# Kernel optimization log

Measured on AMD Instinct MI355X. Metric: run time of the kernel, lower is better.

## Reference

```python
import jax, jax.numpy as jnp
import numpy as np
from jax.ops import segment_sum

N_NODES = 50000
N_EDGES = 800000
HIDDEN = 96
N_CLASSES = 10
N_GRAPHS = 64


def gcn_conv(x, W, b, src, dst, num_nodes):
    """PyG GCNConv: symmetric-normalized aggregation with self-loops.
    out = D^{-1/2} (A + I) D^{-1/2} (x W) + b, with D the degree of A + I.
    Self-loop contribution handled analytically instead of appending edges.
    """
    ones = jnp.ones((src.shape[0],), dtype=x.dtype)
    deg = segment_sum(ones, dst, num_segments=num_nodes) + 1.0  # +1 for self-loop
    dinv = jax.lax.rsqrt(deg)
    h = x @ W  # [N, H] small GEMM
    norm = dinv[src] * dinv[dst]  # [E]
    msg = h[src] * norm[:, None]  # [E, H] dominant gather
    out = segment_sum(msg, dst, num_segments=num_nodes)  # scatter-add
    out = out + h * (dinv * dinv)[:, None]  # self-loop term
    return out + b


def setup_inputs() -> dict:
    key = jax.random.key(0)
    ks = jax.random.split(key, 12)
    x = jax.random.normal(ks[0], (N_NODES, HIDDEN), dtype=jnp.float32)
    edge_index = jax.random.randint(ks[1], (2, N_EDGES), 0, N_NODES, dtype=jnp.int64)
    batch = jnp.sort(jax.random.randint(ks[2], (N_NODES,), 0, N_GRAPHS, dtype=jnp.int64))
    s = 1.0 / np.sqrt(HIDDEN)
    W0 = jax.random.normal(ks[3], (HIDDEN, HIDDEN), dtype=jnp.float32) * s
    b0 = jnp.zeros((HIDDEN,), dtype=jnp.float32)
    W1 = jax.random.normal(ks[4], (HIDDEN, HIDDEN), dtype=jnp.float32) * s
    b1 = jnp.zeros((HIDDEN,), dtype=jnp.float32)
    W2 = jax.random.normal(ks[5], (HIDDEN, HIDDEN), dtype=jnp.float32) * s
    b2 = jnp.zeros((HIDDEN,), dtype=jnp.float32)
    W_lin = jax.random.normal(ks[6], (HIDDEN, N_CLASSES), dtype=jnp.float32) * s
    b_lin = jnp.zeros((N_CLASSES,), dtype=jnp.float32)
    return {"x": x, "edge_index": edge_index, "batch": batch,
            "W0": W0, "b0": b0, "W1": W1, "b1": b1, "W2": W2, "b2": b2,
            "W_lin": W_lin, "b_lin": b_lin}


def reference(x, edge_index, batch, W0, b0, W1, b1, W2, b2, W_lin, b_lin):
    src, dst = edge_index[0], edge_index[1]
    n = x.shape[0]
    h = jax.nn.relu(gcn_conv(x, W0, b0, src, dst, n))
    h = jax.nn.relu(gcn_conv(h, W1, b1, src, dst, n))
    h = gcn_conv(h, W2, b2, src, dst, n)  # last layer: no activation
    # global_mean_pool over batch index
    sums = segment_sum(h, batch, num_segments=N_GRAPHS)  # [G, H]
    cnts = segment_sum(jnp.ones((n,), dtype=h.dtype), batch, num_segments=N_GRAPHS)
    pooled = sums / jnp.maximum(cnts, 1.0)[:, None]
    # dropout is identity in eval mode
    return pooled @ W_lin + b_lin  # [G, num_classes]
```

## Files before the change

### kernel.cpp

```cpp
#include <hip/hip_runtime.h>
#include <hip/hip_bf16.h>

#define HID 96
#define NGRAPHS 64
#define SENT 0xC3C3u
#define NROWS 50116

typedef __attribute__((ext_vector_type(8))) short short8;
typedef __attribute__((ext_vector_type(4))) float floatx4;
typedef __attribute__((ext_vector_type(2))) float floatx2;
typedef __attribute__((ext_vector_type(8))) unsigned short ushort8v;
typedef __attribute__((ext_vector_type(2))) unsigned int uint2v;

__device__ __forceinline__ float bf16_to_f32(unsigned short u) {
    unsigned int v = ((unsigned int)u) << 16;
    return __builtin_bit_cast(float, v);
}
__device__ __forceinline__ unsigned short f32_to_bf16(float f) {
    unsigned int u = __builtin_bit_cast(unsigned int, f);
    u += 0x7fff + ((u >> 16) & 1);
    return (unsigned short)(u >> 16);
}
__device__ __forceinline__ unsigned char f32_to_fp8(float f) {
    return (unsigned char)(__builtin_amdgcn_cvt_pk_fp8_f32(f, f, 0, false) & 0xff);
}
__device__ __forceinline__ void fp8x8_decode(uint2v u, float* __restrict__ o) {
    floatx2 a0 = __builtin_amdgcn_cvt_pk_f32_fp8(u[0], false);
    floatx2 a1 = __builtin_amdgcn_cvt_pk_f32_fp8(u[0], true);
    floatx2 a2 = __builtin_amdgcn_cvt_pk_f32_fp8(u[1], false);
    floatx2 a3 = __builtin_amdgcn_cvt_pk_f32_fp8(u[1], true);
    o[0] = a0[0]; o[1] = a0[1]; o[2] = a1[0]; o[3] = a1[1];
    o[4] = a2[0]; o[5] = a2[1]; o[6] = a3[0]; o[7] = a3[1];
}

__device__ __forceinline__ void gather_core4(
    const unsigned char* __restrict__ h8, const unsigned short* __restrict__ csr,
    int r0, int r1, int r2, int TAIL, int it2, int pe8,
    float* __restrict__ aA, float* __restrict__ aB) {
    int s = r0;
    ushort8v i0 = *(const ushort8v*)(csr + (s < r2 ? s : TAIL));
    ushort8v i1 = *(const ushort8v*)(csr + (s + 8 < r2 ? s + 8 : TAIL));
    for (int it = 0; it < it2; ++it) {
        uint2v v0[8], v1[8];
#pragma unroll
        for (int j = 0; j < 8; ++j)
            v0[j] = *(const uint2v*)(h8 + (int)i0[j] * HID + pe8);
#pragma unroll
        for (int j = 0; j < 8; ++j)
            v1[j] = *(const uint2v*)(h8 + (int)i1[j] * HID + pe8);
        int sn = s + 16;
        ushort8v n0 = *(const ushort8v*)(csr + (sn < r2 ? sn : TAIL));
        ushort8v n1 = *(const ushort8v*)(csr + (sn + 8 < r2 ? sn + 8 : TAIL));
#pragma unroll
        for (int h = 0; h < 4; ++h) {
            float t[8] = {0, 0, 0, 0, 0, 0, 0, 0};
#pragma unroll
            for (int j = 0; j < 4; ++j) {
                float d[8];
                fp8x8_decode((h < 2 ? v0 : v1)[(h & 1) * 4 + j], d);
#pragma unroll
                for (int f = 0; f < 8; ++f) t[f] += d[f];
            }
            int bh = s + h * 4;
            bool bA = bh < r1;
            bool bV = bh < r2;
#pragma unroll
            for (int f = 0; f < 8; ++f) {
                float x = bA ? t[f] : 0.0f;
                float v = bV ? t[f] : 0.0f;
                aA[f] += x;
                aB[f] += v - x;
            }
        }
        i0 = n0;
        i1 = n1;
        s = sn;
    }
}

__global__ __launch_bounds__(256) void init_kernel(
    int* __restrict__ deg, float* __restrict__ psum,
    unsigned char* __restrict__ bufA, unsigned char* __restrict__ bufB, int N,
    int NB, const float* __restrict__ W0, const float* __restrict__ W1,
    const float* __restrict__ W2, unsigned short* __restrict__ Wz) {
    int b = blockIdx.x;
    if (b >= NB) {
        int wsel = b - NB;
        const float* W = (wsel == 0) ? W0 : (wsel == 1) ? W1 : W2;
        unsigned short* dst = Wz + wsel * HID * HID;
        for (int e = threadIdx.x; e < HID * HID; e += blockDim.x) {
            int k = e / HID, n = e % HID;
            int nt = n >> 4, kki = k >> 5, quad = (k >> 3) & 3, j = k & 7;
            int lane = (n & 15) | (quad << 4);
            dst[(((nt * 3 + kki) * 64 + lane) << 3) | j] = f32_to_bf16(W[e]);
        }
        return;
    }
    int i = b * 256 + threadIdx.x;
    if (i < N) deg[i] = 0;
    if (i < NGRAPHS * HID + NGRAPHS) psum[i] = 0.0f;
    if (i < HID) {
        bufA[(size_t)SENT * HID + i] = 0;
        bufB[(size_t)SENT * HID + i] = 0;
    }
}

__global__ void deg_kernel(const int* __restrict__ dst, int* __restrict__ deg,
                           int n_edges) {
    int t = blockIdx.x * blockDim.x + threadIdx.x;
    int e0 = t * 4;
    if (e0 + 4 <= n_edges) {
        int4 d4 = *(const int4*)(dst + e0);
        atomicAdd(&deg[d4.x], 1);
        atomicAdd(&deg[d4.y], 1);
        atomicAdd(&deg[d4.z], 1);
        atomicAdd(&deg[d4.w], 1);
    } else {
        for (int e = e0; e < n_edges; e++) atomicAdd(&deg[dst[e]], 1);
    }
}

__global__ __launch_bounds__(256) void scan_phaseA(const int* __restrict__ deg,
                                                   float* __restrict__ dinv,
                                                   int* __restrict__ blocksum,
                                                   int N) {
    int i = blockIdx.x * 256 + threadIdx.x;
    int d = (i < N) ? deg[i] : 0;
    if (i < N) dinv[i] = rsqrtf((float)d + 1.0f);
    int v = (d + 3) & ~3;
#pragma unroll
    for (int off = 32; off > 0; off >>= 1) v += __shfl_down(v, off, 64);
    __shared__ int s[4];
    if ((threadIdx.x & 63) == 0) s[threadIdx.x >> 6] = v;
    __syncthreads();
    if (threadIdx.x == 0) blocksum[blockIdx.x] = s[0] + s[1] + s[2] + s[3];
}

__global__ __launch_bounds__(256) void scan_phaseC(const int* __restrict__ deg,
                                                   const int* __restrict__ blocksum,
                                                   int* __restrict__ rowptr,
                                                   int* __restrict__ cursor,
                                                   int N, int NB) {
    int t = threadIdx.x;
    int mine = (t < NB && t < blockIdx.x) ? blocksum[t] : 0;
#pragma unroll
    for (int off = 32; off > 0; off >>= 1) mine += __shfl_down(mine, off, 64);
    __shared__ int ps[4];
    if ((t & 63) == 0) ps[t >> 6] = mine;
    __syncthreads();
    int pref = ps[0] + ps[1] + ps[2] + ps[3];

    __shared__ int s[256];
    int i = blockIdx.x * 256 + t;
    int own = (i < N) ? (deg[i] + 3) & ~3 : 0;
    s[t] = own;
    __syncthreads();
#pragma unroll
    for (int off = 1; off < 256; off <<= 1) {
        int v = (t >= off) ? s[t - off] : 0;
        __syncthreads();
        s[t] += v;
        __syncthreads();
    }
    if (i < N) {
        int r = pref + s[t] - own;
        rowptr[i] = r;
        cursor[i] = r;
        if (i == N - 1) rowptr[N] = r + own;
    }
}

__global__ void csr_fill(const int* __restrict__ src, const int* __restrict__ dst,
                         int* __restrict__ cursor,
                         unsigned short* __restrict__ csr_src, int n_edges) {
    int t = blockIdx.x * blockDim.x + threadIdx.x;
    int e0 = t * 8;
    if (e0 + 8 <= n_edges) {
        int4 da = *(const int4*)(dst + e0);
        int4 db = *(const int4*)(dst + e0 + 4);
        int4 sa = *(const int4*)(src + e0);
        int4 sb = *(const int4*)(src + e0 + 4);
        int p0 = atomicAdd(&cursor[da.x], 1);
        int p1 = atomicAdd(&cursor[da.y], 1);
        int p2 = atomicAdd(&cursor[da.z], 1);
        int p3 = atomicAdd(&cursor[da.w], 1);
        int p4 = atomicAdd(&cursor[db.x], 1);
        int p5 = atomicAdd(&cursor[db.y], 1);
        int p6 = atomicAdd(&cursor[db.z], 1);
        int p7 = atomicAdd(&cursor[db.w], 1);
        csr_src[p0] = (unsigned short)sa.x;
        csr_src[p1] = (unsigned short)sa.y;
        csr_src[p2] = (unsigned short)sa.z;
        csr_src[p3] = (unsigned short)sa.w;
        csr_src[p4] = (unsigned short)sb.x;
        csr_src[p5] = (unsigned short)sb.y;
        csr_src[p6] = (unsigned short)sb.z;
        csr_src[p7] = (unsigned short)sb.w;
    } else {
        for (int e = e0; e < n_edges; e++) {
            int p = atomicAdd(&cursor[dst[e]], 1);
            csr_src[p] = (unsigned short)src[e];
        }
    }
}

__global__ __launch_bounds__(256) void gemm0_f32(
    const float* __restrict__ X, const unsigned short* __restrict__ Wz,
    const float* __restrict__ dinv, unsigned char* __restrict__ Out, int Mtiles) {
    int wv = threadIdx.x >> 6;
    int lane = threadIdx.x & 63;
    int quad = lane >> 4;
    int mrow = lane & 15;
    int tt = blockIdx.x * 2 + (wv >> 1);
    int half = wv & 1;
    if (tt >= Mtiles) return;

    short8 bfrag[9];
    const short8* Wz8 = (const short8*)Wz;
#pragma unroll
    for (int f = 0; f < 9; f++) bfrag[f] = Wz8[(half * 9 + f) * 64 + lane];

    int m0 = tt * 16;
    const float* arow = X + (size_t)(m0 + mrow) * HID + quad * 8;
    short8 a[3];
#pragma unroll
    for (int kb = 0; kb < 3; kb++) {
        float4 u = *(const float4*)(arow + kb * 32);
        float4 v = *(const float4*)(arow + kb * 32 + 4);
        short8 t;
        t[0] = (short)f32_to_bf16(u.x); t[1] = (short)f32_to_bf16(u.y);
        t[2] = (short)f32_to_bf16(u.z); t[3] = (short)f32_to_bf16(u.w);
        t[4] = (short)f32_to_bf16(v.x); t[5] = (short)f32_to_bf16(v.y);
        t[6] = (short)f32_to_bf16(v.z); t[7] = (short)f32_to_bf16(v.w);
        a[kb] = t;
    }
    float dscale[4];
#pragma unroll
    for (int r = 0; r < 4; r++) dscale[r] = dinv[m0 + quad * 4 + r];
    unsigned char* orow = Out + (size_t)m0 * HID;
#pragma unroll
    for (int ntl = 0; ntl < 3; ntl++) {
        int nt = half * 3 + ntl;
        floatx4 c = {0.0f, 0.0f, 0.0f, 0.0f};
        c = __builtin_amdgcn_mfma_f32_16x16x32_bf16(a[0], bfrag[ntl * 3 + 0], c, 0, 0, 0);
        c = __builtin_amdgcn_mfma_f32_16x16x32_bf16(a[1], bfrag[ntl * 3 + 1], c, 0, 0, 0);
        c = __builtin_amdgcn_mfma_f32_16x16x32_bf16(a[2], bfrag[ntl * 3 + 2], c, 0, 0, 0);
#pragma unroll
        for (int r = 0; r < 4; r++)
            orow[(size_t)(quad * 4 + r) * HID + nt * 16 + mrow] =
                f32_to_fp8(c[r] * dscale[r]);
    }
}

__global__ __launch_bounds__(256) void fused_gather_gemm(
    const unsigned char* __restrict__ h8, const int* __restrict__ rowptr,
    const unsigned short* __restrict__ csr, const float* __restrict__ dinv,
    const float* __restrict__ bias, const unsigned short* __restrict__ Wz,
    unsigned char* __restrict__ Out, int Mtiles, int N) {
    __shared__ unsigned short tile[2][16][104];
    int wv = threadIdx.x >> 6;
    int lane = threadIdx.x & 63;
    int quad = lane >> 4;
    int mrow = lane & 15;
    int tsel = wv >> 1;
    int half = wv & 1;
    int tt = blockIdx.x * 2 + tsel;
    bool active = tt < Mtiles;
    int g = lane >> 4;
    int p = lane & 15;
    int pe = (p < 12) ? p : 11;
    int pe8 = pe * 8;

    if (active) {
        int TAIL = rowptr[N];
        int j0 = half * 8 + g * 2;
        int na = tt * 16 + j0;
        int r0 = rowptr[na], r1 = rowptr[na + 1], r2 = rowptr[na + 2];
        float da = dinv[na], db = dinv[na + 1];
        float aA[8], aB[8];
        uint2v sva = *(const uint2v*)(h8 + (size_t)na * HID + pe8);
        uint2v svb = *(const uint2v*)(h8 + (size_t)(na + 1) * HID + pe8);
        fp8x8_decode(sva, aA);
        fp8x8_decode(svb, aB);
        int it2 = (r2 - r0 + 15) >> 4;
        int o = __shfl_xor(it2, 16, 64);
        it2 = it2 > o ? it2 : o;
        o = __shfl_xor(it2, 32, 64);
        it2 = it2 > o ? it2 : o;
        gather_core4(h8, csr, r0, r1, r2, TAIL, it2, pe8, aA, aB);
        float4 bb0 = *(const float4*)(bias + pe8);
        float4 bb1 = *(const float4*)(bias + pe8 + 4);
        float bv[8] = {bb0.x, bb0.y, bb0.z, bb0.w, bb1.x, bb1.y, bb1.z, bb1.w};
        if (p < 12) {
            ushort8v oA, oB;
#pragma unroll
            for (int f = 0; f < 8; ++f) {
                oA[f] = f32_to_bf16(fmaxf(aA[f] * da + bv[f], 0.0f));
                oB[f] = f32_to_bf16(fmaxf(aB[f] * db + bv[f], 0.0f));
            }
            *(ushort8v*)(&tile[tsel][j0][pe8]) = oA;
            *(ushort8v*)(&tile[tsel][j0 + 1][pe8]) = oB;
        }
    }
    __syncthreads();
    if (!active) return;

    short8 bfrag[9];
    const short8* Wz8 = (const short8*)Wz;
#pragma unroll
    for (int f = 0; f < 9; f++) bfrag[f] = Wz8[(half * 9 + f) * 64 + lane];

    const unsigned short* tp = &tile[tsel][0][0];
    short8 a[3];
#pragma unroll
    for (int kb = 0; kb < 3; kb++)
        a[kb] = *(const short8*)(tp + mrow * 104 + quad * 8 + kb * 32);
    int n0 = tt * 16;
    float dscale[4];
#pragma unroll
    for (int r = 0; r < 4; r++) dscale[r] = dinv[n0 + quad * 4 + r];
    unsigned char* orow = Out + (size_t)n0 * HID;
#pragma unroll
    for (int ntl = 0; ntl < 3; ntl++) {
        int nt = half * 3 + ntl;
        floatx4 c = {0.0f, 0.0f, 0.0f, 0.0f};
        c = __builtin_amdgcn_mfma_f32_16x16x32_bf16(a[0], bfrag[ntl * 3 + 0], c, 0, 0, 0);
        c = __builtin_amdgcn_mfma_f32_16x16x32_bf16(a[1], bfrag[ntl * 3 + 1], c, 0, 0, 0);
        c = __builtin_amdgcn_mfma_f32_16x16x32_bf16(a[2], bfrag[ntl * 3 + 2], c, 0, 0, 0);
#pragma unroll
        for (int r = 0; r < 4; r++)
            orow[(size_t)(quad * 4 + r) * HID + nt * 16 + mrow] =
                f32_to_fp8(c[r] * dscale[r]);
    }
}

__global__ __launch_bounds__(256) void gather_pool(
    const unsigned char* __restrict__ h8, const int* __restrict__ rowptr,
    const unsigned short* __restrict__ csr, const float* __restrict__ dinv,
    const float* __restrict__ bias, const int* __restrict__ batch,
    float* __restrict__ psum, float* __restrict__ pcnt, int Ntiles8, int N) {
    __shared__ float stage[4][8][96];
    int wv = threadIdx.x >> 6;
    int lane = threadIdx.x & 63;
    int tt = blockIdx.x * 4 + wv;
    if (tt >= Ntiles8) return;
    int g = lane >> 4;
    int p = lane & 15;
    int pe = (p < 12) ? p : 11;
    int pe8 = pe * 8;

    int TAIL = rowptr[N];
    int n0 = tt * 8;
    int na = n0 + g * 2;
    int r0 = rowptr[na], r1 = rowptr[na + 1], r2 = rowptr[na + 2];
    float da = dinv[na], db = dinv[na + 1];
    float aA[8], aB[8];
    uint2v sva = *(const uint2v*)(h8 + (size_t)na * HID + pe8);
    uint2v svb = *(const uint2v*)(h8 + (size_t)(na + 1) * HID + pe8);
    fp8x8_decode(sva, aA);
    fp8x8_decode(svb, aB);
    int it2 = (r2 - r0 + 15) >> 4;
    int o = __shfl_xor(it2, 16, 64);
    it2 = it2 > o ? it2 : o;
    o = __shfl_xor(it2, 32, 64);
    it2 = it2 > o ? it2 : o;
    gather_core4(h8, csr, r0, r1, r2, TAIL, it2, pe8, aA, aB);
    float4 bb0 = *(const float4*)(bias + pe8);
    float4 bb1 = *(const float4*)(bias + pe8 + 4);
    float bv[8] = {bb0.x, bb0.y, bb0.z, bb0.w, bb1.x, bb1.y, bb1.z, bb1.w};
    if (p < 12) {
        floatx4 oa0 = {aA[0] * da + bv[0], aA[1] * da + bv[1],
                       aA[2] * da + bv[2], aA[3] * da + bv[3]};
        floatx4 oa1 = {aA[4] * da + bv[4], aA[5] * da + bv[5],
                       aA[6] * da + bv[6], aA[7] * da + bv[7]};
        floatx4 ob0 = {aB[0] * db + bv[0], aB[1] * db + bv[1],
                       aB[2] * db + bv[2], aB[3] * db + bv[3]};
        floatx4 ob1 = {aB[4] * db + bv[4], aB[5] * db + bv[5],
                       aB[6] * db + bv[6], aB[7] * db + bv[7]};
        *(floatx4*)(&stage[wv][g * 2][pe8]) = oa0;
        *(floatx4*)(&stage[wv][g * 2][pe8 + 4]) = oa1;
        *(floatx4*)(&stage[wv][g * 2 + 1][pe8]) = ob0;
        *(floatx4*)(&stage[wv][g * 2 + 1][pe8 + 4]) = ob1;
    }
    asm volatile("s_waitcnt lgkmcnt(0)" ::: "memory");

    int fi = (lane < 48) ? lane * 2 : 94;
    int g_cur = batch[n0];
    float s0 = 0.0f, s1 = 0.0f;
    int cnt = 0;
#pragma unroll
    for (int j = 0; j < 8; ++j) {
        int gb = batch[n0 + j];
        if (gb != g_cur) {
            if (lane < 48) {
                atomicAdd(&psum[g_cur * HID + fi], s0);
                atomicAdd(&psum[g_cur * HID + fi + 1], s1);
            }
            if (lane == 0) atomicAdd(&pcnt[g_cur], (float)cnt);
            s0 = 0.0f; s1 = 0.0f; cnt = 0;
            g_cur = gb;
        }
        s0 += stage[wv][j][fi];
        s1 += stage[wv][j][fi + 1];
        cnt++;
    }
    if (lane < 48) {
        atomicAdd(&psum[g_cur * HID + fi], s0);
        atomicAdd(&psum[g_cur * HID + fi + 1], s1);
    }
    if (lane == 0) atomicAdd(&pcnt[g_cur], (float)cnt);
}

__global__ __launch_bounds__(640) void final_kernel(
    const float* __restrict__ sums, const float* __restrict__ cnts,
    const float* __restrict__ Wlin, const float* __restrict__ blin,
    float* __restrict__ out) {
    int t = threadIdx.x;
    if (t >= NGRAPHS * 10) return;
    int g = t / 10;
    int c = t % 10;
    float denom = fmaxf(cnts[g], 1.0f);
    float acc = blin[c];
#pragma unroll
    for (int f = 0; f < HID; f++)
        acc += (sums[g * HID + f] / denom) * Wlin[f * 10 + c];
    out[t] = acc;
}

extern "C" void kernel_launch(void* const* d_in, const int* in_sizes, int n_in,
                              void* d_out, int out_size, void* d_ws,
                              size_t ws_size, hipStream_t stream) {
    const float* x = (const float*)d_in[0];
    const int* edge = (const int*)d_in[1];
    const int* batch = (const int*)d_in[2];
    const float* W[3] = {(const float*)d_in[3], (const float*)d_in[5],
                         (const float*)d_in[7]};
    const float* B[3] = {(const float*)d_in[4], (const float*)d_in[6],
                         (const float*)d_in[8]};
    const float* Wlin = (const float*)d_in[9];
    const float* blin = (const float*)d_in[10];
    float* out = (float*)d_out;

    int N = in_sizes[0] / HID;
    int E = in_sizes[1] / 2;
    const int* src = edge;
    const int* dst = edge + E;
    int NB = (N + 255) / 256;

    char* ws = (char*)d_ws;
    size_t off = 0;
    auto alloc = [&](size_t bytes) {
        void* p = ws + off;
        off += (bytes + 255) & ~(size_t)255;
        return p;
    };
    int* deg = (int*)alloc((size_t)N * 4);
    float* dinv = (float*)alloc((size_t)N * 4);
    int* rowptr = (int*)alloc(((size_t)N + 1) * 4);
    int* cursor = (int*)alloc((size_t)N * 4);
    int* blocksum = (int*)alloc((size_t)NB * 4);
    size_t csr_cap = (size_t)E + 4 * (size_t)N;
    unsigned short* csr_src = (unsigned short*)alloc(csr_cap * 2 + 64);
    unsigned short* Wz = (unsigned short*)alloc(3 * HID * HID * 2);
    unsigned char* bufA = (unsigned char*)alloc((size_t)NROWS * HID);
    unsigned char* bufB = (unsigned char*)alloc((size_t)NROWS * HID);
    float* psum = (float*)alloc((NGRAPHS * HID + NGRAPHS) * 4);
    float* pcnt = psum + NGRAPHS * HID;

    hipMemsetAsync(csr_src, 0xC3, csr_cap * 2, stream);
    init_kernel<<<NB + 3, 256, 0, stream>>>(deg, psum, bufA, bufB, N, NB,
                                            W[0], W[1], W[2], Wz);
    deg_kernel<<<(E / 4 + 255) / 256, 256, 0, stream>>>(dst, deg, E);
    scan_phaseA<<<NB, 256, 0, stream>>>(deg, dinv, blocksum, N);
    scan_phaseC<<<NB, 256, 0, stream>>>(deg, blocksum, rowptr, cursor, N, NB);
    csr_fill<<<(E / 8 + 255) / 256, 256, 0, stream>>>(src, dst, cursor, csr_src, E);

    int Mtiles = (N + 15) / 16;
    int grid2 = (Mtiles + 1) / 2;
    int Ntiles8 = (N + 7) / 8;
    int gridp = (Ntiles8 + 3) / 4;

    gemm0_f32<<<grid2, 256, 0, stream>>>(x, Wz, dinv, bufA, Mtiles);
    fused_gather_gemm<<<grid2, 256, 0, stream>>>(
        bufA, rowptr, csr_src, dinv, B[0], Wz + 1 * HID * HID, bufB, Mtiles, N);
    fused_gather_gemm<<<grid2, 256, 0, stream>>>(
        bufB, rowptr, csr_src, dinv, B[1], Wz + 2 * HID * HID, bufA, Mtiles, N);
    gather_pool<<<gridp, 256, 0, stream>>>(bufA, rowptr, csr_src, dinv, B[2],
                                           batch, psum, pcnt, Ntiles8, N);
    final_kernel<<<1, 640, 0, stream>>>(psum, pcnt, Wlin, blin, out);
}
```

Before: 299.7 us.

## Split final-layer features into two planar halves for cache-friendly gather-pool

The second fused gather-GEMM now writes its fp8 output as two planar 48-feature halves instead of 96-wide rows. The final gather+pool kernel runs twice, once per half, so each pass's gather working set (about 2.4MB) fits better in cache. The cost is an extra launch, a second pass over the CSR indices and row pointers, and twice the atomic pooling traffic, with fewer active lanes per wave.

Result: slower. 324.2 us (+8.2%).

```diff
diff --git a/kernel.cpp b/kernel.cpp
--- a/kernel.cpp
+++ b/kernel.cpp
@@ -5,6 +5,7 @@
 #define NGRAPHS 64
 #define SENT 0xC3C3u
 #define NROWS 50116
+#define PLN48 ((size_t)NROWS * 48)
 
 typedef __attribute__((ext_vector_type(8))) short short8;
 typedef __attribute__((ext_vector_type(4))) float floatx4;
@@ -12,10 +13,6 @@
 typedef __attribute__((ext_vector_type(8))) unsigned short ushort8v;
 typedef __attribute__((ext_vector_type(2))) unsigned int uint2v;
 
-__device__ __forceinline__ float bf16_to_f32(unsigned short u) {
-    unsigned int v = ((unsigned int)u) << 16;
-    return __builtin_bit_cast(float, v);
-}
 __device__ __forceinline__ unsigned short f32_to_bf16(float f) {
     unsigned int u = __builtin_bit_cast(unsigned int, f);
     u += 0x7fff + ((u >> 16) & 1);
@@ -33,6 +30,7 @@
     o[4] = a2[0]; o[5] = a2[1]; o[6] = a3[0]; o[7] = a3[1];
 }
 
+template <int RS>
 __device__ __forceinline__ void gather_core4(
     const unsigned char* __restrict__ h8, const unsigned short* __restrict__ csr,
     int r0, int r1, int r2, int TAIL, int it2, int pe8,
@@ -44,10 +42,10 @@
         uint2v v0[8], v1[8];
 #pragma unroll
         for (int j = 0; j < 8; ++j)
-            v0[j] = *(const uint2v*)(h8 + (int)i0[j] * HID + pe8);
+            v0[j] = *(const uint2v*)(h8 + (int)i0[j] * RS + pe8);
 #pragma unroll
         for (int j = 0; j < 8; ++j)
-            v1[j] = *(const uint2v*)(h8 + (int)i1[j] * HID + pe8);
+            v1[j] = *(const uint2v*)(h8 + (int)i1[j] * RS + pe8);
         int sn = s + 16;
         ushort8v n0 = *(const ushort8v*)(csr + (sn < r2 ? sn : TAIL));
         ushort8v n1 = *(const ushort8v*)(csr + (sn + 8 < r2 ? sn + 8 : TAIL));
@@ -80,7 +78,8 @@
 
 __global__ __launch_bounds__(256) void init_kernel(
     int* __restrict__ deg, float* __restrict__ psum,
-    unsigned char* __restrict__ bufA, unsigned char* __restrict__ bufB, int N,
+    unsigned char* __restrict__ bufA, unsigned char* __restrict__ bufB,
+    unsigned char* __restrict__ bufP, int N,
     int NB, const float* __restrict__ W0, const float* __restrict__ W1,
     const float* __restrict__ W2, unsigned short* __restrict__ Wz) {
     int b = blockIdx.x;
@@ -102,6 +101,10 @@
     if (i < HID) {
         bufA[(size_t)SENT * HID + i] = 0;
         bufB[(size_t)SENT * HID + i] = 0;
+    }
+    if (i < 48) {
+        bufP[(size_t)SENT * 48 + i] = 0;
+        bufP[PLN48 + (size_t)SENT * 48 + i] = 0;
     }
 }
 
@@ -256,7 +259,7 @@
     const unsigned char* __restrict__ h8, const int* __restrict__ rowptr,
     const unsigned short* __restrict__ csr, const float* __restrict__ dinv,
     const float* __restrict__ bias, const unsigned short* __restrict__ Wz,
-    unsigned char* __restrict__ Out, int Mtiles, int N) {
+    unsigned char* __restrict__ Out, int Mtiles, int N, int planar) {
     __shared__ unsigned short tile[2][16][104];
     int wv = threadIdx.x >> 6;
     int lane = threadIdx.x & 63;
@@ -287,7 +290,7 @@
         it2 = it2 > o ? it2 : o;
         o = __shfl_xor(it2, 32, 64);
         it2 = it2 > o ? it2 : o;
-        gather_core4(h8, csr, r0, r1, r2, TAIL, it2, pe8, aA, aB);
+        gather_core4<HID>(h8, csr, r0, r1, r2, TAIL, it2, pe8, aA, aB);
         float4 bb0 = *(const float4*)(bias + pe8);
         float4 bb1 = *(const float4*)(bias + pe8 + 4);
         float bv[8] = {bb0.x, bb0.y, bb0.z, bb0.w, bb1.x, bb1.y, bb1.z, bb1.w};
@@ -319,34 +322,50 @@
     float dscale[4];
 #pragma unroll
     for (int r = 0; r < 4; r++) dscale[r] = dinv[n0 + quad * 4 + r];
-    unsigned char* orow = Out + (size_t)n0 * HID;
-#pragma unroll
-    for (int ntl = 0; ntl < 3; ntl++) {
-        int nt = half * 3 + ntl;
-        floatx4 c = {0.0f, 0.0f, 0.0f, 0.0f};
-        c = __builtin_amdgcn_mfma_f32_16x16x32_bf16(a[0], bfrag[ntl * 3 + 0], c, 0, 0, 0);
-        c = __builtin_amdgcn_mfma_f32_16x16x32_bf16(a[1], bfrag[ntl * 3 + 1], c, 0, 0, 0);
-        c = __builtin_amdgcn_mfma_f32_16x16x32_bf16(a[2], bfrag[ntl * 3 + 2], c, 0, 0, 0);
-#pragma unroll
-        for (int r = 0; r < 4; r++)
-            orow[(size_t)(quad * 4 + r) * HID + nt * 16 + mrow] =
-                f32_to_fp8(c[r] * dscale[r]);
-    }
-}
-
-__global__ __launch_bounds__(256) void gather_pool(
-    const unsigned char* __restrict__ h8, const int* __restrict__ rowptr,
+    if (planar) {
+        unsigned char* op = Out + (size_t)half * PLN48 + (size_t)n0 * 48;
+#pragma unroll
+        for (int ntl = 0; ntl < 3; ntl++) {
+            floatx4 c = {0.0f, 0.0f, 0.0f, 0.0f};
+            c = __builtin_amdgcn_mfma_f32_16x16x32_bf16(a[0], bfrag[ntl * 3 + 0], c, 0, 0, 0);
+            c = __builtin_amdgcn_mfma_f32_16x16x32_bf16(a[1], bfrag[ntl * 3 + 1], c, 0, 0, 0);
+            c = __builtin_amdgcn_mfma_f32_16x16x32_bf16(a[2], bfrag[ntl * 3 + 2], c, 0, 0, 0);
+#pragma unroll
+            for (int r = 0; r < 4; r++)
+                op[(size_t)(quad * 4 + r) * 48 + ntl * 16 + mrow] =
+                    f32_to_fp8(c[r] * dscale[r]);
+        }
+    } else {
+        unsigned char* orow = Out + (size_t)n0 * HID;
+#pragma unroll
+        for (int ntl = 0; ntl < 3; ntl++) {
+            int nt = half * 3 + ntl;
+            floatx4 c = {0.0f, 0.0f, 0.0f, 0.0f};
+            c = __builtin_amdgcn_mfma_f32_16x16x32_bf16(a[0], bfrag[ntl * 3 + 0], c, 0, 0, 0);
+            c = __builtin_amdgcn_mfma_f32_16x16x32_bf16(a[1], bfrag[ntl * 3 + 1], c, 0, 0, 0);
+            c = __builtin_amdgcn_mfma_f32_16x16x32_bf16(a[2], bfrag[ntl * 3 + 2], c, 0, 0, 0);
+#pragma unroll
+            for (int r = 0; r < 4; r++)
+                orow[(size_t)(quad * 4 + r) * HID + nt * 16 + mrow] =
+                    f32_to_fp8(c[r] * dscale[r]);
+        }
+    }
+}
+
+__global__ __launch_bounds__(256) void gather_pool_ph(
+    const unsigned char* __restrict__ hp, const int* __restrict__ rowptr,
     const unsigned short* __restrict__ csr, const float* __restrict__ dinv,
     const float* __restrict__ bias, const int* __restrict__ batch,
-    float* __restrict__ psum, float* __restrict__ pcnt, int Ntiles8, int N) {
-    __shared__ float stage[4][8][96];
+    float* __restrict__ psum, float* __restrict__ pcnt, int Ntiles8, int N,
+    int ph) {
+    __shared__ float stage[4][8][48];
     int wv = threadIdx.x >> 6;
     int lane = threadIdx.x & 63;
     int tt = blockIdx.x * 4 + wv;
     if (tt >= Ntiles8) return;
     int g = lane >> 4;
     int p = lane & 15;
-    int pe = (p < 12) ? p : 11;
+    int pe = (p < 6) ? p : 5;
     int pe8 = pe * 8;
 
     int TAIL = rowptr[N];
@@ -355,8 +374,8 @@
     int r0 = rowptr[na], r1 = rowptr[na + 1], r2 = rowptr[na + 2];
     float da = dinv[na], db = dinv[na + 1];
     float aA[8], aB[8];
-    uint2v sva = *(const uint2v*)(h8 + (size_t)na * HID + pe8);
-    uint2v svb = *(const uint2v*)(h8 + (size_t)(na + 1) * HID + pe8);
+    uint2v sva = *(const uint2v*)(hp + (size_t)na * 48 + pe8);
+    uint2v svb = *(const uint2v*)(hp + (size_t)(na + 1) * 48 + pe8);
     fp8x8_decode(sva, aA);
     fp8x8_decode(svb, aB);
     int it2 = (r2 - r0 + 15) >> 4;
@@ -364,11 +383,12 @@
     it2 = it2 > o ? it2 : o;
     o = __shfl_xor(it2, 32, 64);
     it2 = it2 > o ? it2 : o;
-    gather_core4(h8, csr, r0, r1, r2, TAIL, it2, pe8, aA, aB);
-    float4 bb0 = *(const float4*)(bias + pe8);
-    float4 bb1 = *(const float4*)(bias + pe8 + 4);
+    gather_core4<48>(hp, csr, r0, r1, r2, TAIL, it2, pe8, aA, aB);
+    const float* bp = bias + ph * 48 + pe8;
+    float4 bb0 = *(const float4*)(bp);
+    float4 bb1 = *(const float4*)(bp + 4);
     float bv[8] = {bb0.x, bb0.y, bb0.z, bb0.w, bb1.x, bb1.y, bb1.z, bb1.w};
-    if (p < 12) {
+    if (p < 6) {
         floatx4 oa0 = {aA[0] * da + bv[0], aA[1] * da + bv[1],
                        aA[2] * da + bv[2], aA[3] * da + bv[3]};
         floatx4 oa1 = {aA[4] * da + bv[4], aA[5] * da + bv[5],
@@ -384,7 +404,8 @@
     }
     asm volatile("s_waitcnt lgkmcnt(0)" ::: "memory");
 
-    int fi = (lane < 48) ? lane * 2 : 94;
+    int fi = (lane < 24) ? lane * 2 : 46;
+    float* pbase = psum + ph * 48;
     int g_cur = batch[n0];
     float s0 = 0.0f, s1 = 0.0f;
     int cnt = 0;
@@ -392,11 +413,11 @@
     for (int j = 0; j < 8; ++j) {
         int gb = batch[n0 + j];
         if (gb != g_cur) {
-            if (lane < 48) {
-                atomicAdd(&psum[g_cur * HID + fi], s0);
-                atomicAdd(&psum[g_cur * HID + fi + 1], s1);
+            if (lane < 24) {
+                atomicAdd(&pbase[g_cur * HID + fi], s0);
+                atomicAdd(&pbase[g_cur * HID + fi + 1], s1);
             }
-            if (lane == 0) atomicAdd(&pcnt[g_cur], (float)cnt);
+            if (ph == 0 && lane == 0) atomicAdd(&pcnt[g_cur], (float)cnt);
             s0 = 0.0f; s1 = 0.0f; cnt = 0;
             g_cur = gb;
         }
@@ -404,11 +425,11 @@
         s1 += stage[wv][j][fi + 1];
         cnt++;
     }
-    if (lane < 48) {
-        atomicAdd(&psum[g_cur * HID + fi], s0);
-        atomicAdd(&psum[g_cur * HID + fi + 1], s1);
-    }
-    if (lane == 0) atomicAdd(&pcnt[g_cur], (float)cnt);
+    if (lane < 24) {
+        atomicAdd(&pbase[g_cur * HID + fi], s0);
+        atomicAdd(&pbase[g_cur * HID + fi + 1], s1);
+    }
+    if (ph == 0 && lane == 0) atomicAdd(&pcnt[g_cur], (float)cnt);
 }
 
 __global__ __launch_bounds__(640) void final_kernel(
@@ -464,11 +485,12 @@
     unsigned short* Wz = (unsigned short*)alloc(3 * HID * HID * 2);
     unsigned char* bufA = (unsigned char*)alloc((size_t)NROWS * HID);
     unsigned char* bufB = (unsigned char*)alloc((size_t)NROWS * HID);
+    unsigned char* bufP = (unsigned char*)alloc(2 * PLN48);
     float* psum = (float*)alloc((NGRAPHS * HID + NGRAPHS) * 4);
     float* pcnt = psum + NGRAPHS * HID;
 
     hipMemsetAsync(csr_src, 0xC3, csr_cap * 2, stream);
-    init_kernel<<<NB + 3, 256, 0, stream>>>(deg, psum, bufA, bufB, N, NB,
+    init_kernel<<<NB + 3, 256, 0, stream>>>(deg, psum, bufA, bufB, bufP, N, NB,
                                             W[0], W[1], W[2], Wz);
     deg_kernel<<<(E / 4 + 255) / 256, 256, 0, stream>>>(dst, deg, E);
     scan_phaseA<<<NB, 256, 0, stream>>>(deg, dinv, blocksum, N);
@@ -482,10 +504,12 @@
 
     gemm0_f32<<<grid2, 256, 0, stream>>>(x, Wz, dinv, bufA, Mtiles);
     fused_gather_gemm<<<grid2, 256, 0, stream>>>(
-        bufA, rowptr, csr_src, dinv, B[0], Wz + 1 * HID * HID, bufB, Mtiles, N);
+        bufA, rowptr, csr_src, dinv, B[0], Wz + 1 * HID * HID, bufB, Mtiles, N, 0);
     fused_gather_gemm<<<grid2, 256, 0, stream>>>(
-        bufB, rowptr, csr_src, dinv, B[1], Wz + 2 * HID * HID, bufA, Mtiles, N);
-    gather_pool<<<gridp, 256, 0, stream>>>(bufA, rowptr, csr_src, dinv, B[2],
-                                           batch, psum, pcnt, Ntiles8, N);
+        bufB, rowptr, csr_src, dinv, B[1], Wz + 2 * HID * HID, bufP, Mtiles, N, 1);
+    gather_pool_ph<<<gridp, 256, 0, stream>>>(bufP, rowptr, csr_src, dinv, B[2],
+                                              batch, psum, pcnt, Ntiles8, N, 0);
+    gather_pool_ph<<<gridp, 256, 0, stream>>>(bufP + PLN48, rowptr, csr_src, dinv,
+                                              B[2], batch, psum, pcnt, Ntiles8, N, 1);
     final_kernel<<<1, 640, 0, stream>>>(psum, pcnt, Wlin, blin, out);
 }
```
